# Kernel optimization log

Measured on AMD Instinct MI355X. Metric: run time of the kernel, lower is better.

## Reference

```python
import jax, jax.numpy as jnp
import numpy as np

BUCKET = 32   # bucket_size hard-coded in module
HEADS = 8
LN_EPS = 1e-5
SELF_ATTN_VALUE = -5e4  # TOKEN_SELF_ATTN_VALUE from reformer-pytorch


def _layer_norm(x, g, b):
    m = jnp.mean(x, axis=-1, keepdims=True)
    v = jnp.mean((x - m) ** 2, axis=-1, keepdims=True)
    return (x - m) / jnp.sqrt(v + LN_EPS) * g + b


def _lsh_attention(qk, v, rot):
    # qk, v: (B=b*h, T, Dh); rot: (Dh, n_buckets//2); n_hashes = 1
    B, T, D = qk.shape
    n_buckets = T // BUCKET
    # hash: random rotations, argmax over [r, -r]
    r = jnp.einsum('btf,fi->bti', qk, rot)                 # (B, T, n_buckets//2)
    r = jnp.concatenate([r, -r], axis=-1)                  # (B, T, n_buckets)
    buckets = jnp.argmax(r, axis=-1)                       # (B, T) int
    t = jnp.arange(T)
    key = buckets * T + t                                  # unique sort key
    sticker = jnp.argsort(key, axis=-1)                    # (B, T) permutation
    undo = jnp.argsort(sticker, axis=-1)
    sqk = jnp.take_along_axis(qk, sticker[..., None], axis=1)
    sv = jnp.take_along_axis(v, sticker[..., None], axis=1)
    # chunk into n_buckets chunks of size BUCKET
    bq_t = sticker.reshape(B, n_buckets, BUCKET)
    bq = sqk.reshape(B, n_buckets, BUCKET, D)
    bv = sv.reshape(B, n_buckets, BUCKET, D)
    nrm = jnp.sqrt(jnp.sum(bq * bq, axis=-1, keepdims=True))
    bk = bq / jnp.maximum(nrm, 1e-12)                      # shared-QK: keys are unit-norm queries
    def look_one_back(xx):
        return jnp.concatenate([xx, jnp.roll(xx, 1, axis=1)], axis=2)
    bk = look_one_back(bk)
    bvv = look_one_back(bv)
    bkv_t = look_one_back(bq_t)
    dots = jnp.einsum('bcie,bcje->bcij', bq, bk) * (D ** -0.5)  # (B, C, 32, 64)
    self_mask = bq_t[:, :, :, None] == bkv_t[:, :, None, :]
    dots = jnp.where(self_mask, SELF_ATTN_VALUE, dots)
    attn = jax.nn.softmax(dots, axis=-1)
    bo = jnp.einsum('bcij,bcje->bcie', attn, bvv)
    so = bo.reshape(B, T, D)
    return jnp.take_along_axis(so, undo[..., None], axis=1)   # unsort (n_hashes=1 -> probs=1)


def _lsh_self_attention(h, w_qk, w_v, w_out, b_out, rot):
    b, t, d = h.shape
    dh = d // HEADS
    qk = (h @ w_qk).reshape(b, t, HEADS, dh).transpose(0, 2, 1, 3).reshape(b * HEADS, t, dh)
    vv = (h @ w_v).reshape(b, t, HEADS, dh).transpose(0, 2, 1, 3).reshape(b * HEADS, t, dh)
    o = _lsh_attention(qk, vv, rot)
    o = o.reshape(b, HEADS, t, dh).transpose(0, 2, 1, 3).reshape(b, t, d)
    return o @ w_out + b_out


def setup_inputs() -> dict:
    key = jax.random.key(0)
    ks = jax.random.split(key, 8)
    B, T, D, F = 8, 4096, 512, 2048
    dh, nb = D // HEADS, T // BUCKET
    s = 0.02
    return {
        'x': jax.random.normal(ks[0], (B, T, D), jnp.float32),
        'w_qk': jax.random.normal(ks[1], (D, D), jnp.float32) * s,
        'w_v': jax.random.normal(ks[2], (D, D), jnp.float32) * s,
        'w_out': jax.random.normal(ks[3], (D, D), jnp.float32) * s,
        'b_out': jnp.zeros((D,), jnp.float32),
        'ln1_g': jnp.ones((D,), jnp.float32),
        'ln1_b': jnp.zeros((D,), jnp.float32),
        'w_ff1': jax.random.normal(ks[4], (D, F), jnp.float32) * s,
        'b_ff1': jnp.zeros((F,), jnp.float32),
        'w_ff2': jax.random.normal(ks[5], (F, D), jnp.float32) * s,
        'b_ff2': jnp.zeros((D,), jnp.float32),
        'ln2_g': jnp.ones((D,), jnp.float32),
        'ln2_b': jnp.zeros((D,), jnp.float32),
        'rotations': jax.random.normal(ks[6], (dh, nb // 2), jnp.float32),
    }


def reference(x, w_qk, w_v, w_out, b_out, ln1_g, ln1_b, w_ff1, b_ff1,
              w_ff2, b_ff2, ln2_g, ln2_b, rotations):
    # y1 = x + Attn(LN1(x)); y2 = x + FFN(LN2(y1)); out = mean(y1, y2)
    h1 = _layer_norm(x, ln1_g, ln1_b)
    y1 = x + _lsh_self_attention(h1, w_qk, w_v, w_out, b_out, rotations)
    h2 = _layer_norm(y1, ln2_g, ln2_b)
    ffn = jax.nn.relu(h2 @ w_ff1 + b_ff1) @ w_ff2 + b_ff2
    y2 = x + ffn
    return 0.5 * (y1 + y2)
```

## Files before the change

kernel.cpp:

```cpp
#include <hip/hip_runtime.h>
#include <stdint.h>

typedef _Float16 f16;
typedef _Float16 f16x8 __attribute__((ext_vector_type(8)));
typedef float    f32x4 __attribute__((ext_vector_type(4)));
typedef unsigned long long u64;

__device__ __forceinline__ void gload16(const void* g, void* l) {
  __builtin_amdgcn_global_load_lds(
      (__attribute__((address_space(1))) void*)g,
      (__attribute__((address_space(3))) void*)l, 16, 0, 0);
}

#define PH_PRE() \
  __builtin_amdgcn_s_barrier(); \
  asm volatile("s_waitcnt lgkmcnt(0)" ::: "memory"); \
  __builtin_amdgcn_sched_barrier(0); \
  __builtin_amdgcn_s_setprio(1);

#define PH_POST() \
  __builtin_amdgcn_s_setprio(0); \
  __builtin_amdgcn_s_barrier(); \
  __builtin_amdgcn_sched_barrier(0);

#define MFMA_QUAD(q, af) \
  _Pragma("unroll") for (int m2 = 0; m2 < 2; ++m2) \
  _Pragma("unroll") for (int nt = 0; nt < 4; ++nt) \
  _Pragma("unroll") for (int kk = 0; kk < 2; ++kk) \
    acc[(q)*2 + m2][nt] = __builtin_amdgcn_mfma_f32_16x16x32_f16( \
        af[m2][kk], bf[nt][kk], acc[(q)*2 + m2][nt], 0, 0, 0);

#define RD_A(dst, abase, q2) \
  _Pragma("unroll") for (int m2 = 0; m2 < 2; ++m2) \
  _Pragma("unroll") for (int kk = 0; kk < 2; ++kk) { \
    const int lr = (q2)*32 + m2*16 + l15; \
    dst[m2][kk] = *(const f16x8*)&abase[lr*64 + (((kk*4 + l4) ^ (lr & 7)) << 3)]; }

#define RD_B(bbase) \
  _Pragma("unroll") for (int nt = 0; nt < 4; ++nt) \
  _Pragma("unroll") for (int kk = 0; kk < 2; ++kk) { \
    const int lr = brow + nt*16 + l15; \
    bf[nt][kk] = *(const f16x8*)&bbase[lr*64 + (((kk*4 + l4) ^ (lr & 7)) << 3)]; }

template<int EPI>
__global__ __launch_bounds__(512, 2)
void gemm256(const f16* __restrict__ A, int lda,
             const f16* __restrict__ Bt, int ldb,
             int K, int N,
             float* __restrict__ outf, f16* __restrict__ outh,
             f16* __restrict__ outh2,
             const float* __restrict__ bias,
             const float* __restrict__ add1)
{
  __shared__ __align__(16) f16 lds[65536];
  const int tid = threadIdx.x, lane = tid & 63;
  const int wid = tid >> 6;
  const int wm = wid >> 2, wn = wid & 3;
  const int l15 = lane & 15, l4 = lane >> 4;

  const int gx = gridDim.x;
  int lid = blockIdx.y * gx + blockIdx.x;
  const int cpx = (gx * gridDim.y) >> 3;
  lid = (lid & 7) * cpx + (lid >> 3);
  const long bm0 = (long)(lid / gx) * 256;
  const long bn0 = (long)(lid % gx) * 256;

  const int rs = tid >> 3, cs = tid & 7;
  const int cg = cs ^ (rs & 7);
  const int nkt = K >> 6;
  const int nmask = nkt - 1;

  auto stageA = [&](int d, int half, int kt) {
    f16* dst = &lds[(d * 4 + half) * 8192];
    const long kb = (long)kt * 64 + cg * 8;
    const f16* src = A + (bm0 + half * 128) * lda + kb;
#pragma unroll
    for (int rr = 0; rr < 2; ++rr) {
      const int row = rs + rr * 64;
      gload16(src + (long)row * lda, dst + row * 64 + cs * 8);
    }
  };
  auto stageB = [&](int d, int half, int kt) {
    f16* dst = &lds[(d * 4 + 2 + half) * 8192];
    const long kb = (long)kt * 64 + cg * 8;
    const f16* src = Bt + (bn0 + half * 128) * ldb + kb;
#pragma unroll
    for (int rr = 0; rr < 2; ++rr) {
      const int row = rs + rr * 64;
      gload16(src + (long)row * ldb, dst + row * 64 + cs * 8);
    }
  };

  const f16* aBase0 = &lds[(0 + wm) * 8192];
  const f16* aBase1 = &lds[(4 + wm) * 8192];
  const f16* bBase0 = &lds[(2 + (wn >> 1)) * 8192];
  const f16* bBase1 = &lds[(6 + (wn >> 1)) * 8192];
  const int brow = (wn & 1) * 64;

  f32x4 acc[8][4];
#pragma unroll
  for (int i = 0; i < 8; ++i)
#pragma unroll
    for (int j = 0; j < 4; ++j) acc[i][j] = f32x4{0.f, 0.f, 0.f, 0.f};
  f16x8 bf[4][2], afA[2][2], afB[2][2];

  stageB(0, 0, 0); stageB(0, 1, 0); stageA(0, 0, 0); stageA(0, 1, 0);
  asm volatile("s_waitcnt vmcnt(4)" ::: "memory");
  stageB(1, 0, 1); stageB(1, 1, 1); stageA(1, 0, 1);
  asm volatile("s_waitcnt vmcnt(6)" ::: "memory");
  __builtin_amdgcn_s_barrier();
  __builtin_amdgcn_sched_barrier(0);

  for (int j = 0; j < nkt; j += 2) {
    const int t2 = (j + 2) & nmask, t3 = (j + 3) & nmask;
    RD_B(bBase0); RD_A(afA, aBase0, 0);
    stageA(1, 1, (j + 1) & nmask);
    asm volatile("s_waitcnt lgkmcnt(8)" ::: "memory");
    PH_PRE(); MFMA_QUAD(0, afA); PH_POST();
    RD_A(afB, aBase0, 1); RD_A(afA, aBase0, 2);
    stageB(0, 0, t2);
    PH_PRE(); MFMA_QUAD(1, afB); PH_POST();
    RD_A(afB, aBase0, 3);
    stageB(0, 1, t2);
    PH_PRE(); MFMA_QUAD(2, afA); PH_POST();
    stageA(0, 0, t2);
    asm volatile("s_waitcnt vmcnt(6)" ::: "memory");
    PH_PRE(); MFMA_QUAD(3, afB); PH_POST();
    RD_B(bBase1); RD_A(afA, aBase1, 0);
    stageA(0, 1, t2);
    asm volatile("s_waitcnt lgkmcnt(8)" ::: "memory");
    PH_PRE(); MFMA_QUAD(0, afA); PH_POST();
    RD_A(afB, aBase1, 1); RD_A(afA, aBase1, 2);
    stageB(1, 0, t3);
    PH_PRE(); MFMA_QUAD(1, afB); PH_POST();
    RD_A(afB, aBase1, 3);
    stageB(1, 1, t3);
    PH_PRE(); MFMA_QUAD(2, afA); PH_POST();
    stageA(1, 0, t3);
    asm volatile("s_waitcnt vmcnt(6)" ::: "memory");
    PH_PRE(); MFMA_QUAD(3, afB); PH_POST();
  }
  asm volatile("s_waitcnt vmcnt(0)" ::: "memory");

#pragma unroll
  for (int mt = 0; mt < 8; ++mt)
#pragma unroll
    for (int nt = 0; nt < 4; ++nt)
#pragma unroll
      for (int r = 0; r < 4; ++r) {
        const long grow = bm0 + wm * 128 + mt * 16 + l4 * 4 + r;
        const long gcol = bn0 + wn * 64 + nt * 16 + l15;
        const float c = acc[mt][nt][r];
        if constexpr (EPI == 12) {
          const long idx = grow * (long)N + gcol;
          const float t = c + bias[gcol];
          const float xx = add1[idx];
          outh2[idx] = (f16)(t + xx);
          outh[idx]  = (f16)(xx + 0.5f * t);
        } else if constexpr (EPI == 13) {
          const long idx = grow * (long)N + gcol;
          outh[idx] = (f16)fmaxf(c + bias[gcol], 0.f);
        } else if constexpr (EPI == 17) {
          const int bb = (int)(grow >> 12), tt = (int)(grow & 4095);
          const int hcol = (int)(bn0 >> 6) + wn;
          const int is_v = hcol >> 3, h = hcol & 7;
          f16* base = is_v ? outh2 : outh;
          base[(((long)bb * 8 + h) * 4096 + tt) * 64 + nt * 16 + l15] = (f16)c;
        }
      }
}

#define RD2_B(bbase) \
  _Pragma("unroll") for (int nt = 0; nt < 4; ++nt) \
  _Pragma("unroll") for (int kk = 0; kk < 2; ++kk) { \
    const int lr = brow + nt*16 + l15; \
    bf[nt][kk] = *(const f16x8*)&bbase[lr*64 + (((kk*4 + l4) ^ (lr & 7)) << 3)]; }

#define RD2_A(dst, abase, mt) \
  _Pragma("unroll") for (int kk = 0; kk < 2; ++kk) { \
    const int lr = arow + (mt)*16 + l15; \
    dst[kk] = *(const f16x8*)&abase[lr*64 + (((kk*4 + l4) ^ (lr & 7)) << 3)]; }

#define MFMA_Q1(mt, af) \
  _Pragma("unroll") for (int nt = 0; nt < 4; ++nt) \
  _Pragma("unroll") for (int kk = 0; kk < 2; ++kk) \
    acc[mt][nt] = __builtin_amdgcn_mfma_f32_16x16x32_f16( \
        af[kk], bf[nt][kk], acc[mt][nt], 0, 0, 0);

__global__ __launch_bounds__(512, 2)
void ffn2_8ph(const f16* __restrict__ A, const f16* __restrict__ Bt,
              const f16* __restrict__ sxyh, const float* __restrict__ bias,
              float* __restrict__ outf)
{
  __shared__ __align__(16) f16 lds[49152];
  const int tid = threadIdx.x, lane = tid & 63;
  const int wid = tid >> 6;
  const int wm = wid >> 1, wn = wid & 1;
  const int l15 = lane & 15, l4 = lane >> 4;

  const int gx = gridDim.x;
  int lid = blockIdx.y * gx + blockIdx.x;
  const int cpx = (gx * gridDim.y) >> 3;
  lid = (lid & 7) * cpx + (lid >> 3);
  const long bm0 = (long)(lid / gx) * 256;
  const long bn0 = (long)(lid % gx) * 128;

  const int rs = tid >> 3, cs = tid & 7;
  const int cg = cs ^ (rs & 7);
  const int nmask = 31;

  auto stageA = [&](int d, int half, int kt) {
    f16* dst = &lds[(d * 3 + half) * 8192];
    const long kb = (long)kt * 64 + cg * 8;
    const f16* src = A + (bm0 + half * 128) * 2048 + kb;
#pragma unroll
    for (int rr = 0; rr < 2; ++rr) {
      const int row = rs + rr * 64;
      gload16(src + (long)row * 2048, dst + row * 64 + cs * 8);
    }
  };
  auto stageB = [&](int d, int kt) {
    f16* dst = &lds[(d * 3 + 2) * 8192];
    const long kb = (long)kt * 64 + cg * 8;
    const f16* src = Bt + bn0 * 2048 + kb;
#pragma unroll
    for (int rr = 0; rr < 2; ++rr) {
      const int row = rs + rr * 64;
      gload16(src + (long)row * 2048, dst + row * 64 + cs * 8);
    }
  };

  const f16* aBase0 = &lds[(0 + (wm >> 1)) * 8192];
  const f16* aBase1 = &lds[(3 + (wm >> 1)) * 8192];
  const f16* bBase0 = &lds[2 * 8192];
  const f16* bBase1 = &lds[5 * 8192];
  const int arow = (wm & 1) * 64;
  const int brow = wn * 64;

  f32x4 acc[4][4];
#pragma unroll
  for (int i = 0; i < 4; ++i)
#pragma unroll
    for (int j = 0; j < 4; ++j) acc[i][j] = f32x4{0.f, 0.f, 0.f, 0.f};
  f16x8 bf[4][2], afA[2], afB[2];

  stageB(0, 0); stageA(0, 0, 0); stageA(0, 1, 0);
  stageB(1, 1); stageA(1, 0, 1); stageA(1, 1, 1);
  asm volatile("s_waitcnt vmcnt(6)" ::: "memory");
  __builtin_amdgcn_s_barrier();
  __builtin_amdgcn_sched_barrier(0);

  for (int j = 0; j < 32; j += 2) {
    const int t2 = (j + 2) & nmask, t3 = (j + 3) & nmask;
    RD2_B(bBase0); RD2_A(afA, aBase0, 0);
    asm volatile("s_waitcnt lgkmcnt(8)" ::: "memory");
    PH_PRE(); MFMA_Q1(0, afA); PH_POST();
    RD2_A(afB, aBase0, 1); RD2_A(afA, aBase0, 2);
    stageB(0, t2);
    PH_PRE(); MFMA_Q1(1, afB); PH_POST();
    RD2_A(afB, aBase0, 3);
    PH_PRE(); MFMA_Q1(2, afA); PH_POST();
    stageA(0, 0, t2); stageA(0, 1, t2);
    asm volatile("s_waitcnt vmcnt(6)" ::: "memory");
    PH_PRE(); MFMA_Q1(3, afB); PH_POST();
    RD2_B(bBase1); RD2_A(afA, aBase1, 0);
    asm volatile("s_waitcnt lgkmcnt(8)" ::: "memory");
    PH_PRE(); MFMA_Q1(0, afA); PH_POST();
    RD2_A(afB, aBase1, 1); RD2_A(afA, aBase1, 2);
    stageB(1, t3);
    PH_PRE(); MFMA_Q1(1, afB); PH_POST();
    RD2_A(afB, aBase1, 3);
    PH_PRE(); MFMA_Q1(2, afA); PH_POST();
    stageA(1, 0, t3); stageA(1, 1, t3);
    asm volatile("s_waitcnt vmcnt(6)" ::: "memory");
    PH_PRE(); MFMA_Q1(3, afB); PH_POST();
  }
  asm volatile("s_waitcnt vmcnt(0)" ::: "memory");

#pragma unroll
  for (int mt = 0; mt < 4; ++mt)
#pragma unroll
    for (int nt = 0; nt < 4; ++nt)
#pragma unroll
      for (int r = 0; r < 4; ++r) {
        const long grow = bm0 + wm * 64 + mt * 16 + l4 * 4 + r;
        const long gcol = bn0 + wn * 64 + nt * 16 + l15;
        const long idx = grow * 512 + gcol;
        outf[idx] = (float)sxyh[idx] + 0.5f * (acc[mt][nt][r] + bias[gcol]);
      }
}

__global__ __launch_bounds__(256)
void ln_kernel(const float* __restrict__ in, const float* __restrict__ gam,
               const float* __restrict__ bet, f16* __restrict__ out,
               int ldo, int split)
{
  const long row = (long)blockIdx.x * 4 + (threadIdx.x >> 6);
  const int lane = threadIdx.x & 63;
  const float4* p = (const float4*)(in + row * 512);
  const float4 a = p[lane * 2], b = p[lane * 2 + 1];
  float xv[8] = {a.x, a.y, a.z, a.w, b.x, b.y, b.z, b.w};
  float s = 0.f;
#pragma unroll
  for (int i = 0; i < 8; ++i) s += xv[i];
#pragma unroll
  for (int m = 32; m; m >>= 1) s += __shfl_xor(s, m);
  const float mean = s * (1.f / 512.f);
  float vs = 0.f;
#pragma unroll
  for (int i = 0; i < 8; ++i) { const float d = xv[i] - mean; vs += d * d; }
#pragma unroll
  for (int m = 32; m; m >>= 1) vs += __shfl_xor(vs, m);
  const float rstd = 1.f / sqrtf(vs * (1.f / 512.f) + 1e-5f);
  const float4* gp = (const float4*)gam;
  const float4* bp = (const float4*)bet;
  const float4 g0 = gp[lane * 2], g1 = gp[lane * 2 + 1];
  const float4 b0 = bp[lane * 2], b1 = bp[lane * 2 + 1];
  const float gg[8] = {g0.x, g0.y, g0.z, g0.w, g1.x, g1.y, g1.z, g1.w};
  const float bb[8] = {b0.x, b0.y, b0.z, b0.w, b1.x, b1.y, b1.z, b1.w};
  f16x8 vh, vl;
#pragma unroll
  for (int i = 0; i < 8; ++i) {
    const float y = (xv[i] - mean) * rstd * gg[i] + bb[i];
    const f16 hi = (f16)y;
    vh[i] = hi;
    vl[i] = (f16)((y - (float)hi) * 64.f);
  }
  f16* o = out + row * ldo + lane * 8;
  *(f16x8*)o = vh;
  if (split) *(f16x8*)(o + 512) = vl;
}

__global__ __launch_bounds__(256)
void ln16_kernel(const f16* __restrict__ in, const float* __restrict__ gam,
                 const float* __restrict__ bet, f16* __restrict__ out)
{
  const long row = (long)blockIdx.x * 4 + (threadIdx.x >> 6);
  const int lane = threadIdx.x & 63;
  const f16x8 v = *(const f16x8*)(in + row * 512 + lane * 8);
  float xv[8];
#pragma unroll
  for (int i = 0; i < 8; ++i) xv[i] = (float)v[i];
  float s = 0.f;
#pragma unroll
  for (int i = 0; i < 8; ++i) s += xv[i];
#pragma unroll
  for (int m = 32; m; m >>= 1) s += __shfl_xor(s, m);
  const float mean = s * (1.f / 512.f);
  float vs = 0.f;
#pragma unroll
  for (int i = 0; i < 8; ++i) { const float d = xv[i] - mean; vs += d * d; }
#pragma unroll
  for (int m = 32; m; m >>= 1) vs += __shfl_xor(vs, m);
  const float rstd = 1.f / sqrtf(vs * (1.f / 512.f) + 1e-5f);
  const float4* gp = (const float4*)gam;
  const float4* bp = (const float4*)bet;
  const float4 g0 = gp[lane * 2], g1 = gp[lane * 2 + 1];
  const float4 b0 = bp[lane * 2], b1 = bp[lane * 2 + 1];
  const float gg[8] = {g0.x, g0.y, g0.z, g0.w, g1.x, g1.y, g1.z, g1.w};
  const float bb[8] = {b0.x, b0.y, b0.z, b0.w, b1.x, b1.y, b1.z, b1.w};
  f16x8 vh;
#pragma unroll
  for (int i = 0; i < 8; ++i)
    vh[i] = (f16)((xv[i] - mean) * rstd * gg[i] + bb[i]);
  *(f16x8*)(out + row * 512 + lane * 8) = vh;
}

__global__ __launch_bounds__(256)
void transpose_f16(const float* __restrict__ src, f16* __restrict__ dst, int K, int N)
{
  __shared__ float tile[32][33];
  const int tx = threadIdx.x & 31, ty = threadIdx.x >> 5;
  const long k0 = (long)blockIdx.y * 32, n0 = (long)blockIdx.x * 32;
#pragma unroll
  for (int i = 0; i < 4; ++i)
    tile[ty + i * 8][tx] = src[(k0 + ty + i * 8) * N + n0 + tx];
  __syncthreads();
#pragma unroll
  for (int i = 0; i < 4; ++i)
    dst[(n0 + ty + i * 8) * K + k0 + tx] = (f16)tile[tx][ty + i * 8];
}

__global__ __launch_bounds__(256)
void whash_f32(const float* __restrict__ wqk, const float* __restrict__ rot,
               float* __restrict__ WrT, f16* __restrict__ rotTh)
{
  if (blockIdx.x == 0 && blockIdx.y == 0) {
    for (int idx = threadIdx.x; idx < 4096; idx += 256) {
      const int d = idx >> 6, i = idx & 63;
      rotTh[i * 64 + d] = (f16)rot[idx];
    }
  }
  const int kk = blockIdx.x;
  const int n  = blockIdx.y * 256 + threadIdx.x;
  const int h = n >> 6, i = n & 63;
  float s = 0.f;
  for (int d = 0; d < 64; ++d)
    s += wqk[kk * 512 + h * 64 + d] * rot[d * 64 + i];
  WrT[(long)n * 512 + kk] = s;
}

__global__ __launch_bounds__(256)
void rhash4_kernel(const f16* __restrict__ gqk, const f16* __restrict__ rotTh,
                   int* __restrict__ buckets)
{
  const int tid = threadIdx.x, lane = tid & 63, w = tid >> 6;
  const int bh = blockIdx.x >> 5, tb = blockIdx.x & 31;
  const int t0 = tb * 128;
  const int l15 = lane & 15, l4 = lane >> 4;

  f16x8 br[2][4];
#pragma unroll
  for (int kk = 0; kk < 2; ++kk)
#pragma unroll
    for (int nt = 0; nt < 4; ++nt)
      br[kk][nt] = *(const f16x8*)&rotTh[(nt * 16 + l15) * 64 + kk * 32 + l4 * 8];

  const f16* gqb = gqk + ((long)bh * 4096 + t0) * 64;
  f16x8 aq[2][2];
#pragma unroll
  for (int kk = 0; kk < 2; ++kk)
#pragma unroll
    for (int mt = 0; mt < 2; ++mt)
      aq[kk][mt] = *(const f16x8*)&gqb[(long)(w * 32 + mt * 16 + l15) * 64 + kk * 32 + l4 * 8];

  f32x4 acc[2][4];
#pragma unroll
  for (int i = 0; i < 2; ++i)
#pragma unroll
    for (int j = 0; j < 4; ++j) acc[i][j] = f32x4{0.f, 0.f, 0.f, 0.f};
#pragma unroll
  for (int kk = 0; kk < 2; ++kk)
#pragma unroll
    for (int mt = 0; mt < 2; ++mt)
#pragma unroll
      for (int nt = 0; nt < 4; ++nt)
        acc[mt][nt] = __builtin_amdgcn_mfma_f32_16x16x32_f16(aq[kk][mt], br[kk][nt], acc[mt][nt], 0, 0, 0);

#pragma unroll
  for (int mt = 0; mt < 2; ++mt)
#pragma unroll
    for (int r = 0; r < 4; ++r) {
      const float v0 = acc[mt][0][r], v1 = acc[mt][1][r];
      const float v2 = acc[mt][2][r], v3 = acc[mt][3][r];
      unsigned int k0 = (__float_as_uint(fabsf(v0)) & ~63u) | (unsigned int)(63 - l15);
      unsigned int k1 = (__float_as_uint(fabsf(v1)) & ~63u) | (unsigned int)(47 - l15);
      unsigned int k2 = (__float_as_uint(fabsf(v2)) & ~63u) | (unsigned int)(31 - l15);
      unsigned int k3 = (__float_as_uint(fabsf(v3)) & ~63u) | (unsigned int)(15 - l15);
      float ss = v0 * v0 + v1 * v1 + v2 * v2 + v3 * v3;
#pragma unroll
      for (int m = 1; m < 16; m <<= 1) ss += __shfl_xor(ss, m);

      unsigned int mk = max(max(k0, k1), max(k2, k3));
#pragma unroll
      for (int m = 1; m < 16; m <<= 1) mk = max(mk, (unsigned int)__shfl_xor((int)mk, m));
      const unsigned int key1 = mk;
      const int col1 = 63 - (int)(key1 & 63u);
      const float m1f = __uint_as_float(key1 & ~63u);
      const int nt1 = col1 >> 4;
      const float vsel = (nt1 == 0) ? v0 : (nt1 == 1) ? v1 : (nt1 == 2) ? v2 : v3;
      const bool owner = (col1 & 15) == l15;
      const u64 bal = __ballot(owner && (vsel < 0.f));
      const int neg = (int)((bal >> (l4 * 16 + (col1 & 15))) & 1ull);
      const int bucket = col1 + (neg << 6);
      if (owner) {
        if (nt1 == 0) k0 = 0; else if (nt1 == 1) k1 = 0;
        else if (nt1 == 2) k2 = 0; else k3 = 0;
      }
      mk = max(max(k0, k1), max(k2, k3));
#pragma unroll
      for (int m = 1; m < 16; m <<= 1) mk = max(mk, (unsigned int)__shfl_xor((int)mk, m));
      const int col2 = 63 - (int)(mk & 63u);
      const float m2f = __uint_as_float(mk & ~63u);
      {
        const int nt2 = col2 >> 4;
        if ((col2 & 15) == l15) {
          if (nt2 == 0) k0 = 0; else if (nt2 == 1) k1 = 0;
          else if (nt2 == 2) k2 = 0; else k3 = 0;
        }
      }
      mk = max(max(k0, k1), max(k2, k3));
#pragma unroll
      for (int m = 1; m < 16; m <<= 1) mk = max(mk, (unsigned int)__shfl_xor((int)mk, m));
      const int col3 = 63 - (int)(mk & 63u);

      if (l15 == 0) {
        const int row = w * 32 + mt * 16 + l4 * 4 + r;
        const int bht = bh * 4096 + t0 + row;
        const float margin = m1f - m2f;
        const float rms = sqrtf(ss * (1.f / 64.f));
        const int flag = (margin < 0.015f * rms) ? 1 : 0;
        buckets[bht] = bucket | (col2 << 8) | (col3 << 16) | (flag << 24);
      }
    }
}

__global__ __launch_bounds__(256)
void fixup2_kernel(const f16* __restrict__ hsplit, const float* __restrict__ WrT,
                   int* __restrict__ buckets)
{
  const int wid = (blockIdx.x * 256 + threadIdx.x) >> 6;
  const int lane = threadIdx.x & 63;
  for (int batch = 0; batch < 4; ++batch) {
    const int base = wid * 256 + batch * 64;
    const int packed = buckets[base + lane];
    u64 bal = __ballot((packed >> 24) & 1);
    while (bal) {
      const int i = (int)__ffsll((long long)bal) - 1;
      bal &= bal - 1;
      const int row = base + i;
      const int pk = __shfl(packed, i);
      const int h = (row >> 12) & 7;
      const long hrow = (long)(row >> 15) * 4096 + (row & 4095);
      const f16* hp = hsplit + hrow * 1024 + lane * 8;
      const f16x8 hi = *(const f16x8*)hp;
      const f16x8 lo = *(const f16x8*)(hp + 512);
      float h1[8];
#pragma unroll
      for (int k = 0; k < 8; ++k) h1[k] = (float)hi[k] + (float)lo[k] * 0.015625f;
      const int cols[3] = { pk & 63, (pk >> 8) & 63, (pk >> 16) & 63 };
      float best = -1e30f; int bi = 999;
#pragma unroll
      for (int c = 0; c < 3; ++c) {
        const int cc = cols[c];
        const float* wp = WrT + ((long)(h * 64 + cc)) * 512 + lane * 8;
        const float4 w0 = *(const float4*)wp;
        const float4 w1 = *(const float4*)(wp + 4);
        float s = h1[0] * w0.x + h1[1] * w0.y + h1[2] * w0.z + h1[3] * w0.w
                + h1[4] * w1.x + h1[5] * w1.y + h1[6] * w1.z + h1[7] * w1.w;
#pragma unroll
        for (int m = 32; m; m >>= 1) s += __shfl_xor(s, m);
        if (s > best || (s == best && cc < bi)) { best = s; bi = cc; }
        const float ns = -s; const int ni = 64 + cc;
        if (ns > best || (ns == best && ni < bi)) { best = ns; bi = ni; }
      }
      if (lane == 0) buckets[row] = bi;
    }
  }
}

__global__ __launch_bounds__(256)
void sort_kernel(const int* __restrict__ buckets, int* __restrict__ sticker)
{
  __shared__ int bkt[4096];
  __shared__ unsigned int cnts[64][128];
  __shared__ unsigned char rnk[4096];
  __shared__ int tot[128];
  __shared__ int base[128];
  const int bh = blockIdx.x;
  const int tid = threadIdx.x;
  const int lane = tid & 63, wv = tid >> 6;

  for (int i = tid; i < 4096; i += 256) bkt[i] = buckets[(long)bh * 4096 + i] & 127;
  for (int i = tid; i < 64 * 128; i += 256) ((unsigned int*)cnts)[i] = 0u;
  __syncthreads();

  for (int it = 0; it < 16; ++it) {
    const int c = wv * 16 + it;
    const int t = c * 64 + lane;
    const int b = bkt[t];
    unsigned long long m = ~0ull;
#pragma unroll
    for (int k = 0; k < 7; ++k) {
      const bool bit = (b >> k) & 1;
      const unsigned long long bal = __ballot(bit);
      m &= bit ? bal : ~bal;
    }
    const int rk = (int)__popcll(m & ((1ull << lane) - 1ull));
    rnk[t] = (unsigned char)rk;
    if (rk == 0) cnts[c][b] = (unsigned int)__popcll(m);
  }
  __syncthreads();

  if (tid < 128) {
    unsigned int run = 0;
    for (int c = 0; c < 64; ++c) {
      const unsigned int x = cnts[c][tid];
      cnts[c][tid] = run;
      run += x;
    }
    tot[tid] = (int)run;
  }
  __syncthreads();
  if (tid == 0) {
    int run = 0;
    for (int b = 0; b < 128; ++b) { base[b] = run; run += tot[b]; }
  }
  __syncthreads();

  for (int it = 0; it < 16; ++it) {
    const int c = wv * 16 + it;
    const int t = c * 64 + lane;
    const int b = bkt[t];
    const int pos = base[b] + (int)cnts[c][b] + (int)rnk[t];
    sticker[(long)bh * 4096 + pos] = t;
  }
}

__global__ __launch_bounds__(256)
void attn2_kernel(const f16* __restrict__ gqk, const f16* __restrict__ gv,
                  const int* __restrict__ sticker, f16* __restrict__ o)
{
  __shared__ __align__(16) f16 sqk[160 * 64];
  __shared__ __align__(16) f16 sVT[64 * 168];
  __shared__ __align__(16) f16 sP[4][32 * 72];
  __shared__ float rnorm[160];
  __shared__ int st[160];

  const int tid = threadIdx.x, lane = tid & 63, w = tid >> 6;
  const int cg = blockIdx.x, bh = blockIdx.y;
  const int b = bh >> 3, h = bh & 7;
  const int p0 = cg * 128 - 32;
  const int l15 = lane & 15, l4 = lane >> 4;

  if (tid < 160) st[tid] = sticker[(long)bh * 4096 + ((p0 + tid) & 4095)] & 4095;
  __syncthreads();

  const f16* gqb = gqk + (long)bh * 4096 * 64;
#pragma unroll
  for (int it = 0; it < 5; ++it) {
    const int idx = it * 256 + tid;
    const int row = idx >> 3, ch = idx & 7;
    const int gsrc = ch ^ (row & 7);
    gload16(gqb + (long)st[row] * 64 + gsrc * 8, &sqk[idx * 8]);
  }

  const f16* gvb = gv + (long)bh * 4096 * 64;
  f16x8 va[5];
#pragma unroll
  for (int i = 0; i < 5; ++i) {
    const int row = w * 40 + i * 8 + (lane >> 3);
    va[i] = *(const f16x8*)&gvb[(long)st[row] * 64 + (lane & 7) * 8];
  }
#pragma unroll
  for (int i = 0; i < 5; ++i) {
    const int row = w * 40 + i * 8 + (lane >> 3);
    const int d0 = (lane & 7) * 8;
#pragma unroll
    for (int e = 0; e < 8; ++e) sVT[(d0 + e) * 168 + row] = va[i][e];
  }
  __syncthreads();

  if (tid < 160) {
    float s = 0.f;
#pragma unroll
    for (int g = 0; g < 8; ++g) {
      const f16x8 v = *(const f16x8*)&sqk[tid * 64 + ((g ^ (tid & 7)) << 3)];
#pragma unroll
      for (int e = 0; e < 8; ++e) { const float f = (float)v[e]; s += f * f; }
    }
    rnorm[tid] = 1.f / fmaxf(sqrtf(s), 1e-12f);
  }
  __syncthreads();

  f32x4 acc[2][4];
#pragma unroll
  for (int i = 0; i < 2; ++i)
#pragma unroll
    for (int j = 0; j < 4; ++j) acc[i][j] = f32x4{0.f, 0.f, 0.f, 0.f};

#pragma unroll
  for (int kk = 0; kk < 2; ++kk) {
    f16x8 aq[2], bk[4];
#pragma unroll
    for (int mt = 0; mt < 2; ++mt) {
      const int row = 32 + w * 32 + mt * 16 + l15;
      const int g = kk * 4 + l4;
      aq[mt] = *(const f16x8*)&sqk[row * 64 + ((g ^ (row & 7)) << 3)];
    }
#pragma unroll
    for (int nt = 0; nt < 4; ++nt) {
      const int row = w * 32 + nt * 16 + l15;
      const int g = kk * 4 + l4;
      bk[nt] = *(const f16x8*)&sqk[row * 64 + ((g ^ (row & 7)) << 3)];
    }
#pragma unroll
    for (int mt = 0; mt < 2; ++mt)
#pragma unroll
      for (int nt = 0; nt < 4; ++nt)
        acc[mt][nt] = __builtin_amdgcn_mfma_f32_16x16x32_f16(aq[mt], bk[nt], acc[mt][nt], 0, 0, 0);
  }

  float rn[4];
#pragma unroll
  for (int nt = 0; nt < 4; ++nt) rn[nt] = rnorm[w * 32 + nt * 16 + l15];

  float pinv[2][4];
#pragma unroll
  for (int mt = 0; mt < 2; ++mt)
#pragma unroll
    for (int r = 0; r < 4; ++r) {
      const int row_i = mt * 16 + l4 * 4 + r;
      float mx = -1e30f;
#pragma unroll
      for (int nt = 0; nt < 4; ++nt) {
        float v = acc[mt][nt][r] * 0.125f * rn[nt];
        if (nt * 16 + l15 == row_i + 32) v = -5e4f;
        acc[mt][nt][r] = v;
        mx = fmaxf(mx, v);
      }
#pragma unroll
      for (int m = 8; m; m >>= 1) mx = fmaxf(mx, __shfl_xor(mx, m));
      float ssum = 0.f;
#pragma unroll
      for (int nt = 0; nt < 4; ++nt) {
        const float pe = expf(acc[mt][nt][r] - mx);
        ssum += pe;
        sP[w][row_i * 72 + nt * 16 + l15] = (f16)pe;
      }
#pragma unroll
      for (int m = 8; m; m >>= 1) ssum += __shfl_xor(ssum, m);
      pinv[mt][r] = 1.f / ssum;
    }
  __syncthreads();

  f32x4 pacc[2][4];
#pragma unroll
  for (int i = 0; i < 2; ++i)
#pragma unroll
    for (int j = 0; j < 4; ++j) pacc[i][j] = f32x4{0.f, 0.f, 0.f, 0.f};

#pragma unroll
  for (int kk = 0; kk < 2; ++kk) {
    f16x8 ap[2], bv[4];
#pragma unroll
    for (int mt = 0; mt < 2; ++mt)
      ap[mt] = *(const f16x8*)&sP[w][(mt * 16 + l15) * 72 + kk * 32 + l4 * 8];
#pragma unroll
    for (int nt = 0; nt < 4; ++nt)
      bv[nt] = *(const f16x8*)&sVT[(nt * 16 + l15) * 168 + w * 32 + kk * 32 + l4 * 8];
#pragma unroll
    for (int mt = 0; mt < 2; ++mt)
#pragma unroll
      for (int nt = 0; nt < 4; ++nt)
        pacc[mt][nt] = __builtin_amdgcn_mfma_f32_16x16x32_f16(ap[mt], bv[nt], pacc[mt][nt], 0, 0, 0);
  }

  const long ob = (long)b * 4096 * 512 + h * 64;
#pragma unroll
  for (int mt = 0; mt < 2; ++mt)
#pragma unroll
    for (int r = 0; r < 4; ++r) {
      const int row_i = mt * 16 + l4 * 4 + r;
      const long t = st[32 + w * 32 + row_i];
      const float sc = pinv[mt][r];
#pragma unroll
      for (int nt = 0; nt < 4; ++nt)
        o[ob + t * 512 + nt * 16 + l15] = (f16)(pacc[mt][nt][r] * sc);
    }
}

extern "C" void kernel_launch(void* const* d_in, const int* in_sizes, int n_in,
                              void* d_out, int out_size, void* d_ws, size_t ws_size,
                              hipStream_t stream)
{
  const float* x     = (const float*)d_in[0];
  const float* w_qk  = (const float*)d_in[1];
  const float* w_v   = (const float*)d_in[2];
  const float* w_out = (const float*)d_in[3];
  const float* b_out = (const float*)d_in[4];
  const float* ln1g  = (const float*)d_in[5];
  const float* ln1b  = (const float*)d_in[6];
  const float* w_ff1 = (const float*)d_in[7];
  const float* b_ff1 = (const float*)d_in[8];
  const float* w_ff2 = (const float*)d_in[9];
  const float* b_ff2 = (const float*)d_in[10];
  const float* ln2g  = (const float*)d_in[11];
  const float* ln2b  = (const float*)d_in[12];
  const float* rot   = (const float*)d_in[13];
  float* out = (float*)d_out;

  char* ws = (char*)d_ws;
  f16* hsplit = (f16*)ws;
  f16* o_buf  = (f16*)ws;
  f16* h2     = (f16*)ws;
  f16* sxy    = (f16*)(ws + 33554432);
  f16* gqk    = (f16*)(ws + 67108864);
  f16* gv     = (f16*)(ws + 100663296);
  f16* y1h    = (f16*)(ws + 67108864);
  f16* abuf   = (f16*)(ws + 67108864);
  char* W0 = ws + 134217728;
  f16* wqkvT = (f16*)W0;
  f16* woutT = (f16*)(W0 + 1048576);
  f16* wff1T = (f16*)(W0 + 1572864);
  f16* wff2T = (f16*)(W0 + 3670016);
  float* WrT = (float*)(W0 + 5767168);
  int* buckets = (int*)(W0 + 6815744);
  int* sticker = (int*)(W0 + 7864320);
  f16* rotTh   = (f16*)(W0 + 8912896);

  const dim3 b256(256);
  const dim3 b512(512);
  transpose_f16<<<dim3(16, 16), b256, 0, stream>>>(w_qk,  wqkvT,             512, 512);
  transpose_f16<<<dim3(16, 16), b256, 0, stream>>>(w_v,   wqkvT + 512 * 512, 512, 512);
  transpose_f16<<<dim3(16, 16), b256, 0, stream>>>(w_out, woutT,             512, 512);
  transpose_f16<<<dim3(64, 16), b256, 0, stream>>>(w_ff1, wff1T,             512, 2048);
  transpose_f16<<<dim3(16, 64), b256, 0, stream>>>(w_ff2, wff2T,             2048, 512);
  whash_f32<<<dim3(512, 2), b256, 0, stream>>>(w_qk, rot, WrT, rotTh);
  ln_kernel<<<dim3(8192), b256, 0, stream>>>(x, ln1g, ln1b, hsplit, 1024, 1);
  gemm256<17><<<dim3(4, 128), b512, 0, stream>>>(hsplit, 1024, wqkvT, 512, 512, 1024,
      nullptr, gqk, gv, nullptr, nullptr);
  rhash4_kernel<<<dim3(2048), b256, 0, stream>>>(gqk, rotTh, buckets);
  fixup2_kernel<<<dim3(256), b256, 0, stream>>>(hsplit, WrT, buckets);
  sort_kernel<<<dim3(64), b256, 0, stream>>>(buckets, sticker);
  attn2_kernel<<<dim3(32, 64), b256, 0, stream>>>(gqk, gv, sticker, o_buf);
  gemm256<12><<<dim3(2, 128), b512, 0, stream>>>(o_buf, 512, woutT, 512, 512, 512,
      nullptr, sxy, y1h, b_out, x);
  ln16_kernel<<<dim3(8192), b256, 0, stream>>>(y1h, ln2g, ln2b, h2);
  for (int c = 0; c < 2; ++c) {
    const long roff = (long)c * 16384;
    gemm256<13><<<dim3(8, 64), b512, 0, stream>>>(h2 + roff * 512, 512, wff1T, 512,
        512, 2048, nullptr, abuf, nullptr, b_ff1, nullptr);
    ffn2_8ph<<<dim3(4, 64), b512, 0, stream>>>(abuf, wff2T, sxy + roff * 512,
        b_ff2, out + roff * 512);
  }
}
```

Baseline: 437.3 us.

## Store fp16 residual copy of x and recompute LN1 in hash fixup

LN1 now writes a plain fp16 normalized output plus an fp16 copy of x, instead of a hi/lo split fp16 pair. The out-projection epilogue reads the fp16 x copy rather than fp32 x, halving that residual read. The fixup kernel now recomputes LayerNorm from fp32 x for the flagged rows, so it no longer needs the low-order half. This cuts memory traffic in the LN and out-proj epilogue, but the residual x is held in fp16, which loses precision.

```diff
diff --git a/kernel.cpp b/kernel.cpp
--- a/kernel.cpp
+++ b/kernel.cpp
@@ -50,7 +50,7 @@
              float* __restrict__ outf, f16* __restrict__ outh,
              f16* __restrict__ outh2,
              const float* __restrict__ bias,
-             const float* __restrict__ add1)
+             const f16* __restrict__ xh)
 {
   __shared__ __align__(16) f16 lds[65536];
   const int tid = threadIdx.x, lane = tid & 63;
@@ -154,7 +154,7 @@
         if constexpr (EPI == 12) {
           const long idx = grow * (long)N + gcol;
           const float t = c + bias[gcol];
-          const float xx = add1[idx];
+          const float xx = (float)xh[idx];
           outh2[idx] = (f16)(t + xx);
           outh[idx]  = (f16)(xx + 0.5f * t);
         } else if constexpr (EPI == 13) {
@@ -291,9 +291,9 @@
 }
 
 __global__ __launch_bounds__(256)
-void ln_kernel(const float* __restrict__ in, const float* __restrict__ gam,
-               const float* __restrict__ bet, f16* __restrict__ out,
-               int ldo, int split)
+void ln_x16_kernel(const float* __restrict__ in, const float* __restrict__ gam,
+                   const float* __restrict__ bet, f16* __restrict__ hh,
+                   f16* __restrict__ xh)
 {
   const long row = (long)blockIdx.x * 4 + (threadIdx.x >> 6);
   const int lane = threadIdx.x & 63;
@@ -318,17 +318,14 @@
   const float4 b0 = bp[lane * 2], b1 = bp[lane * 2 + 1];
   const float gg[8] = {g0.x, g0.y, g0.z, g0.w, g1.x, g1.y, g1.z, g1.w};
   const float bb[8] = {b0.x, b0.y, b0.z, b0.w, b1.x, b1.y, b1.z, b1.w};
-  f16x8 vh, vl;
+  f16x8 vh, vx;
 #pragma unroll
   for (int i = 0; i < 8; ++i) {
-    const float y = (xv[i] - mean) * rstd * gg[i] + bb[i];
-    const f16 hi = (f16)y;
-    vh[i] = hi;
-    vl[i] = (f16)((y - (float)hi) * 64.f);
-  }
-  f16* o = out + row * ldo + lane * 8;
-  *(f16x8*)o = vh;
-  if (split) *(f16x8*)(o + 512) = vl;
+    vh[i] = (f16)((xv[i] - mean) * rstd * gg[i] + bb[i]);
+    vx[i] = (f16)xv[i];
+  }
+  *(f16x8*)(hh + row * 512 + lane * 8) = vh;
+  *(f16x8*)(xh + row * 512 + lane * 8) = vx;
 }
 
 __global__ __launch_bounds__(256)
@@ -496,7 +493,8 @@
 }
 
 __global__ __launch_bounds__(256)
-void fixup2_kernel(const f16* __restrict__ hsplit, const float* __restrict__ WrT,
+void fixup2_kernel(const float* __restrict__ x, const float* __restrict__ gam,
+                   const float* __restrict__ bet, const float* __restrict__ WrT,
                    int* __restrict__ buckets)
 {
   const int wid = (blockIdx.x * 256 + threadIdx.x) >> 6;
@@ -512,12 +510,30 @@
       const int pk = __shfl(packed, i);
       const int h = (row >> 12) & 7;
       const long hrow = (long)(row >> 15) * 4096 + (row & 4095);
-      const f16* hp = hsplit + hrow * 1024 + lane * 8;
-      const f16x8 hi = *(const f16x8*)hp;
-      const f16x8 lo = *(const f16x8*)(hp + 512);
+      const float4* xp = (const float4*)(x + hrow * 512 + lane * 8);
+      const float4 a = xp[0], b = xp[1];
+      float xv[8] = {a.x, a.y, a.z, a.w, b.x, b.y, b.z, b.w};
+      float s = 0.f;
+#pragma unroll
+      for (int k = 0; k < 8; ++k) s += xv[k];
+#pragma unroll
+      for (int m = 32; m; m >>= 1) s += __shfl_xor(s, m);
+      const float mean = s * (1.f / 512.f);
+      float vs = 0.f;
+#pragma unroll
+      for (int k = 0; k < 8; ++k) { const float d = xv[k] - mean; vs += d * d; }
+#pragma unroll
+      for (int m = 32; m; m >>= 1) vs += __shfl_xor(vs, m);
+      const float rstd = 1.f / sqrtf(vs * (1.f / 512.f) + 1e-5f);
+      const float4* gp = (const float4*)(gam + lane * 8);
+      const float4* bp = (const float4*)(bet + lane * 8);
+      const float4 g0 = gp[0], g1 = gp[1];
+      const float4 bb0 = bp[0], bb1 = bp[1];
+      const float gg[8] = {g0.x, g0.y, g0.z, g0.w, g1.x, g1.y, g1.z, g1.w};
+      const float bb[8] = {bb0.x, bb0.y, bb0.z, bb0.w, bb1.x, bb1.y, bb1.z, bb1.w};
       float h1[8];
 #pragma unroll
-      for (int k = 0; k < 8; ++k) h1[k] = (float)hi[k] + (float)lo[k] * 0.015625f;
+      for (int k = 0; k < 8; ++k) h1[k] = (xv[k] - mean) * rstd * gg[k] + bb[k];
       const int cols[3] = { pk & 63, (pk >> 8) & 63, (pk >> 16) & 63 };
       float best = -1e30f; int bi = 999;
 #pragma unroll
@@ -526,12 +542,12 @@
         const float* wp = WrT + ((long)(h * 64 + cc)) * 512 + lane * 8;
         const float4 w0 = *(const float4*)wp;
         const float4 w1 = *(const float4*)(wp + 4);
-        float s = h1[0] * w0.x + h1[1] * w0.y + h1[2] * w0.z + h1[3] * w0.w
-                + h1[4] * w1.x + h1[5] * w1.y + h1[6] * w1.z + h1[7] * w1.w;
-#pragma unroll
-        for (int m = 32; m; m >>= 1) s += __shfl_xor(s, m);
-        if (s > best || (s == best && cc < bi)) { best = s; bi = cc; }
-        const float ns = -s; const int ni = 64 + cc;
+        float sdot = h1[0] * w0.x + h1[1] * w0.y + h1[2] * w0.z + h1[3] * w0.w
+                   + h1[4] * w1.x + h1[5] * w1.y + h1[6] * w1.z + h1[7] * w1.w;
+#pragma unroll
+        for (int m = 32; m; m >>= 1) sdot += __shfl_xor(sdot, m);
+        if (sdot > best || (sdot == best && cc < bi)) { best = sdot; bi = cc; }
+        const float ns = -sdot; const int ni = 64 + cc;
         if (ns > best || (ns == best && ni < bi)) { best = ns; bi = ni; }
       }
       if (lane == 0) buckets[row] = bi;
@@ -771,9 +787,10 @@
   float* out = (float*)d_out;
 
   char* ws = (char*)d_ws;
-  f16* hsplit = (f16*)ws;
+  f16* hh     = (f16*)ws;
   f16* o_buf  = (f16*)ws;
   f16* h2     = (f16*)ws;
+  f16* xh     = (f16*)(ws + 33554432);
   f16* sxy    = (f16*)(ws + 33554432);
   f16* gqk    = (f16*)(ws + 67108864);
   f16* gv     = (f16*)(ws + 100663296);
@@ -797,15 +814,15 @@
   transpose_f16<<<dim3(64, 16), b256, 0, stream>>>(w_ff1, wff1T,             512, 2048);
   transpose_f16<<<dim3(16, 64), b256, 0, stream>>>(w_ff2, wff2T,             2048, 512);
   whash_f32<<<dim3(512, 2), b256, 0, stream>>>(w_qk, rot, WrT, rotTh);
-  ln_kernel<<<dim3(8192), b256, 0, stream>>>(x, ln1g, ln1b, hsplit, 1024, 1);
-  gemm256<17><<<dim3(4, 128), b512, 0, stream>>>(hsplit, 1024, wqkvT, 512, 512, 1024,
+  ln_x16_kernel<<<dim3(8192), b256, 0, stream>>>(x, ln1g, ln1b, hh, xh);
+  gemm256<17><<<dim3(4, 128), b512, 0, stream>>>(hh, 512, wqkvT, 512, 512, 1024,
       nullptr, gqk, gv, nullptr, nullptr);
   rhash4_kernel<<<dim3(2048), b256, 0, stream>>>(gqk, rotTh, buckets);
-  fixup2_kernel<<<dim3(256), b256, 0, stream>>>(hsplit, WrT, buckets);
+  fixup2_kernel<<<dim3(256), b256, 0, stream>>>(x, ln1g, ln1b, WrT, buckets);
   sort_kernel<<<dim3(64), b256, 0, stream>>>(buckets, sticker);
   attn2_kernel<<<dim3(32, 64), b256, 0, stream>>>(gqk, gv, sticker, o_buf);
   gemm256<12><<<dim3(2, 128), b512, 0, stream>>>(o_buf, 512, woutT, 512, 512, 512,
-      nullptr, sxy, y1h, b_out, x);
+      nullptr, sxy, y1h, b_out, xh);
   ln16_kernel<<<dim3(8192), b256, 0, stream>>>(y1h, ln2g, ln2b, h2);
   for (int c = 0; c < 2; ++c) {
     const long roff = (long)c * 16384;
```

New measurement: 440.6 us. About the same (+0.8%).
